# Kernel tuning notes

Hardware: AMD Instinct MI355X
Metric: run time of the kernel (lower is better)

Reference implementation:

```python
import jax, jax.numpy as jnp
import numpy as np

DIM = 512
NUM_HEADS = 8
HEAD_DIM = DIM // NUM_HEADS
GAMMA = 1.0


def setup_inputs() -> dict:
    key = jax.random.key(0)
    ks = jax.random.split(key, 10)
    B, S = 2, 2048
    x_real = jax.random.normal(ks[0], (B, S, DIM), dtype=jnp.float32)
    x_imag = jax.random.normal(ks[1], (B, S, DIM), dtype=jnp.float32)
    def xavier(k, fan_in, fan_out):
        lim = float(np.sqrt(6.0 / (fan_in + fan_out)))
        return jax.random.uniform(k, (fan_in, fan_out), jnp.float32, -lim, lim)
    # torch Linear(in,out): weight [out,in]; we store transposed [in,out]
    Wq = xavier(ks[2], 2 * DIM, DIM); bq = jnp.zeros((DIM,), jnp.float32)
    Wk = xavier(ks[3], 2 * DIM, DIM); bk = jnp.zeros((DIM,), jnp.float32)
    Wv = xavier(ks[4], 2 * DIM, DIM); bv = jnp.zeros((DIM,), jnp.float32)
    Wo = xavier(ks[5], DIM, 2 * DIM); bo = jnp.zeros((2 * DIM,), jnp.float32)
    return {"x_real": x_real, "x_imag": x_imag, "Wq": Wq, "bq": bq,
            "Wk": Wk, "bk": bk, "Wv": Wv, "bv": bv, "Wo": Wo, "bo": bo}


def reference(x_real, x_imag, Wq, bq, Wk, bk, Wv, bv, Wo, bo):
    B, S, _ = x_real.shape
    real_embed = jnp.concatenate([x_real, x_imag], axis=-1)  # [B,S,2*dim]
    def proj(W, b):
        y = real_embed @ W + b                               # [B,S,dim]
        return y.reshape(B, S, NUM_HEADS, HEAD_DIM).transpose(0, 2, 1, 3)  # [B,H,S,d]
    Q = proj(Wq, bq)
    K = proj(Wk, bk)
    V = proj(Wv, bv)
    # softmax over head_dim is broadcast-invariant, so the Bhattacharyya
    # coefficient sum_d sqrt(p_i[d]*q_j[d]) factorizes into a matmul.
    sp = jnp.sqrt(jax.nn.softmax(Q, axis=-1))  # [B,H,S,d]
    sq = jnp.sqrt(jax.nn.softmax(K, axis=-1))  # [B,H,S,d]
    bc = jnp.einsum('bhid,bhjd->bhij', sp, sq)  # Bhattacharyya coeff [B,H,S,S]
    bc = jnp.clip(bc, -1.0, 1.0)
    dist = jnp.arccos(bc)
    attn = jax.nn.softmax(-GAMMA * dist * dist, axis=-1)  # [B,H,S,S]
    attended = jnp.einsum('bhij,bhjd->bhid', attn, V)
    attended = attended.transpose(0, 2, 1, 3).reshape(B, S, DIM)
    out = attended @ Wo + bo  # [B,S,2*dim] = concat(real_out, imag_out)
    return out
```

## Files before the change

### kernel.cpp

```cpp
#include <hip/hip_runtime.h>
#include <math.h>


typedef __attribute__((ext_vector_type(8))) short short8;
typedef __attribute__((ext_vector_type(4))) short bf16x4;
typedef __attribute__((ext_vector_type(4))) float f32x4;
typedef __attribute__((ext_vector_type(2))) float f32x2;
typedef __attribute__((ext_vector_type(4))) unsigned int u32x4;

#define MFMA(a, b, c) __builtin_amdgcn_mfma_f32_16x16x32_bf16((a), (b), (c), 0, 0, 0)

static __device__ __forceinline__ short f2bf(float f) {
    unsigned u = __float_as_uint(f);
    u += 0x7fffu + ((u >> 16) & 1u);
    return (short)(u >> 16);
}

static __device__ __forceinline__ void gld_lds16(const short* g, short* l) {
    __builtin_amdgcn_global_load_lds(
        (const __attribute__((address_space(1))) unsigned int*)g,
        (__attribute__((address_space(3))) unsigned int*)l, 16, 0, 0);
}

__global__ __launch_bounds__(256) void prep_all(
    const float* __restrict__ xr, const float* __restrict__ xi,
    short* __restrict__ xb,
    const float* __restrict__ Wq, const float* __restrict__ Wk,
    const float* __restrict__ Wv, const float* __restrict__ Wo,
    short* __restrict__ wqt, short* __restrict__ wot)
{
    const int bid = blockIdx.x;
    if (bid < 2048) {
        const unsigned wid = bid * 256 + threadIdx.x;
        const int p  = wid & 7;
        const int rp = (wid >> 3) & 31;
        const int kt = (wid >> 8) & 31;
        const int mb = wid >> 13;
        const int up = p ^ (rp & 7);
        const int m  = (mb << 6) | (rp << 1) | (up >> 2);
        const int k  = (kt << 5) | ((up & 3) << 3);
        const float* s = (k < 512) ? (xr + (size_t)m * 512 + k)
                                   : (xi + (size_t)m * 512 + (k - 512));
        float4 t0 = *(const float4*)(s);
        float4 t1 = *(const float4*)(s + 4);
        short8 o;
        o[0] = f2bf(t0.x); o[1] = f2bf(t0.y); o[2] = f2bf(t0.z); o[3] = f2bf(t0.w);
        o[4] = f2bf(t1.x); o[5] = f2bf(t1.y); o[6] = f2bf(t1.z); o[7] = f2bf(t1.w);
        *(short8*)(xb + (size_t)wid * 8) = o;
    } else {
        __shared__ float tt[32][33];
        const int t = bid - 2048;
        const int z = t >> 9;
        const int idx = t & 511;
        const float* src = (z == 0) ? Wq : (z == 1) ? Wk : (z == 2) ? Wv : Wo;
        const int N = (z < 3) ? 512 : 1024;
        const int bx = (z < 3) ? (idx & 15) : (idx & 31);
        const int by = (z < 3) ? (idx >> 4) : (idx >> 5);
        const int n0 = bx << 5, k0 = by << 5;
        const int tx = threadIdx.x & 31, ty = threadIdx.x >> 5;
        #pragma unroll
        for (int i = 0; i < 4; ++i)
            tt[ty + 8 * i][tx] = src[(size_t)(k0 + ty + 8 * i) * N + n0 + tx];
        __syncthreads();
        const int k = k0 + tx;
        const int kt = k >> 5, u = (k >> 3) & 3, off = k & 7;
        #pragma unroll
        for (int i = 0; i < 4; ++i) {
            const int n = n0 + ty + 8 * i;
            const int nb = n >> 6, rn = n & 63;
            const int rp = rn >> 1;
            const int up = ((rn & 1) << 2) | u;
            const int p  = up ^ (rp & 7);
            const float v = tt[tx][ty + 8 * i];
            if (z < 3)
                wqt[(size_t)z * 524288 +
                    ((size_t)(nb * 32 + kt)) * 2048 + rp * 64 + p * 8 + off] = f2bf(v);
            else
                wot[((size_t)(nb * 16 + kt)) * 2048 + rp * 64 + p * 8 + off] = f2bf(v);
        }
    }
}

__global__ __launch_bounds__(64) void qkv_mfma(
    const short* __restrict__ xb, const short* __restrict__ wcat,
    const float* __restrict__ bq, const float* __restrict__ bk,
    const float* __restrict__ bv,
    short* __restrict__ sp, short* __restrict__ sq, short* __restrict__ vt)
{
    __shared__ short As[3][64 * 32];
    __shared__ short Bs[3][64 * 32];
    const int jb = blockIdx.x;
    const int mb = blockIdx.y;
    const int m0 = mb << 6;
    const int lane = threadIdx.x;
    const int l = lane & 15, quad = lane >> 4;
    const int l7 = l & 7;

    const short* gA = xb   + (size_t)mb * 65536 + lane * 8;
    const short* gB = wcat + (size_t)jb * 65536 + lane * 8;

    auto STAGE = [&](int bb, int kk) {
        const int k0 = kk << 11;
        #pragma unroll
        for (int t = 0; t < 4; ++t) {
            gld_lds16(gA + k0 + t * 512, &As[bb][t << 9]);
            gld_lds16(gB + k0 + t * 512, &Bs[bb][t << 9]);
        }
    };

    STAGE(0, 0);
    STAGE(1, 1);
    asm volatile("s_waitcnt vmcnt(8)" ::: "memory");

    const f32x4 z4 = {0.f, 0.f, 0.f, 0.f};
    f32x4 acc[4][4];
    #pragma unroll
    for (int i = 0; i < 4; ++i)
        #pragma unroll
        for (int j = 0; j < 4; ++j) acc[i][j] = z4;

    const int rbase = (l >> 1) << 6;
    const int pA = (((((l & 1) << 2) | quad) ^ ((l >> 1) & 7)) << 3);
    const int rdo = rbase + pA;

    int cb = 0, sb = 2;
    #pragma unroll 1
    for (int kt = 0; kt < 32; ++kt) {
        STAGE(sb, (kt + 2) & 31);
        const short* Al = &As[cb][0];
        const short* Bl = &Bs[cb][0];
        short8 af[4], bfr[4];
        #pragma unroll
        for (int i = 0; i < 4; ++i)
            af[i] = *(const short8*)(Al + (i << 9) + rdo);
        #pragma unroll
        for (int j = 0; j < 4; ++j)
            bfr[j] = *(const short8*)(Bl + (j << 9) + rdo);
        #pragma unroll
        for (int i = 0; i < 4; ++i)
            #pragma unroll
            for (int j = 0; j < 4; ++j)
                acc[i][j] = MFMA(af[i], bfr[j], acc[i][j]);
        asm volatile("s_waitcnt vmcnt(8)" ::: "memory");
        cb = (cb == 2) ? 0 : cb + 1;
        sb = (sb == 2) ? 0 : sb + 1;
    }

    const int op = jb >> 3;
    const int h  = jb & 7;

    if (op < 2) {
        short* dst = (op == 0) ? sp : sq;
        const float* bias = (op == 0) ? bq : bk;
        float bcol[4];
        #pragma unroll
        for (int nt = 0; nt < 4; ++nt) bcol[nt] = bias[(h << 6) + (nt << 4) + l];
        #pragma unroll
        for (int i = 0; i < 4; ++i) {
            #pragma unroll
            for (int reg = 0; reg < 4; ++reg) {
                const int r = m0 + (i << 4) + (quad << 2) + reg;
                const int b = r >> 11, s = r & 2047;
                float v[4];
                #pragma unroll
                for (int nt = 0; nt < 4; ++nt) v[nt] = acc[i][nt][reg] + bcol[nt];
                float mx = fmaxf(fmaxf(v[0], v[1]), fmaxf(v[2], v[3]));
                #pragma unroll
                for (int msk = 1; msk < 16; msk <<= 1) mx = fmaxf(mx, __shfl_xor(mx, msk));
                float e[4], ssum = 0.f;
                #pragma unroll
                for (int nt = 0; nt < 4; ++nt) { e[nt] = __expf(v[nt] - mx); ssum += e[nt]; }
                #pragma unroll
                for (int msk = 1; msk < 16; msk <<= 1) ssum += __shfl_xor(ssum, msk);
                float inv = 1.0f / ssum;
                short* o = dst + ((size_t)((b << 3) + h) * 2048 + s) * 64;
                if (op == 0) {
                    #pragma unroll
                    for (int nt = 0; nt < 4; ++nt)
                        o[(nt << 4) + l] = f2bf(sqrtf(e[nt] * inv));
                } else {
                    const int s7 = r & 7;
                    #pragma unroll
                    for (int nt = 0; nt < 4; ++nt)
                        o[((((nt << 1) + (l >> 3)) ^ s7) << 3) + l7] =
                            f2bf(sqrtf(e[nt] * inv));
                }
            }
        }
    } else {
        float bcol[4];
        #pragma unroll
        for (int nt = 0; nt < 4; ++nt) bcol[nt] = bv[(h << 6) + (nt << 4) + l];
        #pragma unroll
        for (int i = 0; i < 4; ++i) {
            const int sb2 = m0 + (i << 4) + (quad << 2);
            const int b = sb2 >> 11, s = sb2 & 2047;
            const int gg = (s >> 2) & 15;
            const int u = ((gg >> 3) << 2) + (gg & 3);
            const int colp = (s & ~63) + (((u ^ l7)) << 3) + (((gg >> 2) & 1) << 2);
            #pragma unroll
            for (int nt = 0; nt < 4; ++nt) {
                const int d = (nt << 4) + l;
                bf16x4 pk;
                #pragma unroll
                for (int reg = 0; reg < 4; ++reg)
                    pk[reg] = f2bf(acc[i][nt][reg] + bcol[nt]);
                *(bf16x4*)(vt + ((size_t)((b << 3) + h) * 64 + d) * 2048 + colp) = pk;
            }
        }
    }
}

__global__ __launch_bounds__(256, 4) void attn_mfma(
    const short* __restrict__ sp, const short* __restrict__ sq,
    const short* __restrict__ vt,
    float* __restrict__ pnum, float* __restrict__ pden)
{
    __shared__ __align__(16) short sqT[2][64 * 64];
    __shared__ __align__(16) short vtT[2][64 * 64];
    const int bh = blockIdx.y;
    const int m0 = blockIdx.x << 6;
    const int z  = blockIdx.z;
    const int tid = threadIdx.x;
    const int w = tid >> 6, lane = tid & 63;
    const int l = lane & 15, quad = lane >> 4;
    const int l7 = l & 7;

    const short* spB = sp + (size_t)bh * 2048 * 64;
    const short* sqB = sq + (size_t)bh * 2048 * 64;
    const short* vtB = vt + (size_t)bh * 64 * 2048;

    const short* apr = spB + (size_t)(m0 + w * 16 + l) * 64 + quad * 8;
    short8 nq0 = (*(const short8*)(apr)) ^ (short)0x8000;
    short8 nq1 = (*(const short8*)(apr + 32)) ^ (short)0x8000;

    const int lr = lane >> 3;
    const int lu = lane & 7;
    const int r0 = w << 1;

    auto STAGEATT = [&](int buf, int jrow) {
        #pragma unroll
        for (int k = 0; k < 2; ++k) {
            const int r = r0 + k;
            gld_lds16(sqB + (size_t)(jrow + (r << 3) + lr) * 64 + (lu << 3),
                      &sqT[buf][r << 9]);
            gld_lds16(vtB + (size_t)((r << 3) + lr) * 2048 + jrow + (lu << 3),
                      &vtT[buf][r << 9]);
        }
    };

    const int sRd = (quad ^ l7) << 3;

    STAGEATT(0, z << 9);
    __syncthreads();

    const f32x4 ones4 = {1.f, 1.f, 1.f, 1.f};
    const f32x4 z4 = {0.f, 0.f, 0.f, 0.f};
    f32x4 acc[4] = {z4, z4, z4, z4};
    f32x2 den2 = {0.f, 0.f};

    #pragma unroll 1
    for (int jtl = 0; jtl < 8; ++jtl) {
        const int cb = jtl & 1, nb = cb ^ 1;
        const int j0n = ((z << 3) + ((jtl + 1) & 7)) << 6;
        STAGEATT(nb, j0n);

        uint2 pk[4];
        const short* sqL = &sqT[cb][0];
        #pragma unroll
        for (int nt = 0; nt < 4; ++nt) {
            const short* ar = sqL + ((nt * 16 + l) << 6);
            short8 sa0 = *(const short8*)(ar + sRd);
            short8 sa1 = *(const short8*)(ar + (sRd ^ 32));
            f32x4 p = MFMA(sa0, nq0, ones4);
            p = MFMA(sa1, nq1, p);
            f32x2 u01 = {p[0], p[1]};
            f32x2 u23 = {p[2], p[3]};
            const f32x2 zz = {0.f, 0.f};
#if __has_builtin(__builtin_elementwise_max)
            u01 = __builtin_elementwise_max(u01, zz);
            u23 = __builtin_elementwise_max(u23, zz);
#else
            u01.x = fmaxf(u01.x, 0.f); u01.y = fmaxf(u01.y, 0.f);
            u23.x = fmaxf(u23.x, 0.f); u23.y = fmaxf(u23.y, 0.f);
#endif
            f32x2 t01 = {-0.00133017f, -0.00133017f};
            f32x2 t23 = t01;
            t01 = t01 * u01 - 0.00219618f;  t23 = t23 * u23 - 0.00219618f;
            t01 = t01 * u01 - 0.00555151f;  t23 = t23 * u23 - 0.00555151f;
            t01 = t01 * u01 - 0.01465597f;  t23 = t23 * u23 - 0.01465597f;
            t01 = t01 * u01 - 0.04121986f;  t23 = t23 * u23 - 0.04121986f;
            t01 = t01 * u01 - 0.12823956f;  t23 = t23 * u23 - 0.12823956f;
            t01 = t01 * u01 - 0.48089834f;  t23 = t23 * u23 - 0.48089834f;
            t01 = t01 * u01 - 2.88539008f;  t23 = t23 * u23 - 2.88539008f;
            f32x2 w01 = u01 * t01;
            f32x2 w23 = u23 * t23;
#if __has_builtin(__builtin_amdgcn_exp2f)
            float e0 = __builtin_amdgcn_exp2f(w01.x);
            float e1 = __builtin_amdgcn_exp2f(w01.y);
            float e2 = __builtin_amdgcn_exp2f(w23.x);
            float e3 = __builtin_amdgcn_exp2f(w23.y);
#else
            float e0 = exp2f(w01.x), e1 = exp2f(w01.y);
            float e2 = exp2f(w23.x), e3 = exp2f(w23.y);
#endif
            f32x2 es = {e0 + e2, e1 + e3};
            den2 += es;
            pk[nt].x = (__float_as_uint(e0) >> 16) | (__float_as_uint(e1) & 0xffff0000u);
            pk[nt].y = (__float_as_uint(e2) >> 16) | (__float_as_uint(e3) & 0xffff0000u);
        }

        u32x4 c0; c0.x = pk[0].x; c0.y = pk[0].y; c0.z = pk[1].x; c0.w = pk[1].y;
        u32x4 c1; c1.x = pk[2].x; c1.y = pk[2].y; c1.z = pk[3].x; c1.w = pk[3].y;
        short8 pa0 = __builtin_bit_cast(short8, c0);
        short8 pa1 = __builtin_bit_cast(short8, c1);
        const short* vL = &vtT[cb][0];
        #pragma unroll
        for (int t4 = 0; t4 < 4; ++t4) {
            const short* vr = vL + ((t4 * 16 + l) << 6);
            short8 vb0 = *(const short8*)(vr + sRd);
            short8 vb1 = *(const short8*)(vr + (sRd ^ 32));
            acc[t4] = MFMA(pa0, vb0, acc[t4]);
            acc[t4] = MFMA(pa1, vb1, acc[t4]);
        }

        __syncthreads();
    }

    float den = den2.x + den2.y;
    den += __shfl_xor(den, 16);
    den += __shfl_xor(den, 32);
    if (lane < 16)
        pden[(size_t)z * 32768 + bh * 2048 + m0 + w * 16 + l] = den;

    const int b = bh >> 3, hh = bh & 7;
    float* np = pnum + (size_t)z * 4096 * 512;
    #pragma unroll
    for (int t4 = 0; t4 < 4; ++t4)
        #pragma unroll
        for (int reg = 0; reg < 4; ++reg) {
            const int row = m0 + w * 16 + quad * 4 + reg;
            np[((size_t)(b * 2048 + row)) * 512 + hh * 64 + t4 * 16 + l] =
                acc[t4][reg];
        }
}

__global__ __launch_bounds__(256) void combine_attn(
    const float* __restrict__ pnum, const float* __restrict__ pden,
    short* __restrict__ attB)
{
    const int idx = (blockIdx.x * 256 + threadIdx.x) << 3;
    const int r = idx >> 9;
    const int c = idx & 511;
    const int hh = c >> 6;
    const int bh = ((r >> 11) << 3) + hh;
    const int srow = r & 2047;
    float d = 0.f;
    #pragma unroll
    for (int zi = 0; zi < 4; ++zi)
        d += pden[(size_t)zi * 32768 + bh * 2048 + srow];
    const float inv = 1.0f / d;
    float4 a0 = {0.f, 0.f, 0.f, 0.f}, a1 = {0.f, 0.f, 0.f, 0.f};
    #pragma unroll
    for (int zi = 0; zi < 4; ++zi) {
        const float* n0 = pnum + (size_t)zi * 4096 * 512 + (size_t)r * 512 + c;
        float4 b0 = *(const float4*)(n0);
        float4 b1 = *(const float4*)(n0 + 4);
        a0.x += b0.x; a0.y += b0.y; a0.z += b0.z; a0.w += b0.w;
        a1.x += b1.x; a1.y += b1.y; a1.z += b1.z; a1.w += b1.w;
    }
    short8 o;
    o[0] = f2bf(a0.x * inv); o[1] = f2bf(a0.y * inv);
    o[2] = f2bf(a0.z * inv); o[3] = f2bf(a0.w * inv);
    o[4] = f2bf(a1.x * inv); o[5] = f2bf(a1.y * inv);
    o[6] = f2bf(a1.z * inv); o[7] = f2bf(a1.w * inv);
    const int mb = r >> 6, rm = r & 63;
    const int kt = c >> 5, u = (c >> 3) & 3;
    const int rp = rm >> 1;
    const int up = ((rm & 1) << 2) | u;
    const int p  = up ^ (rp & 7);
    *(short8*)(attB + ((size_t)(mb * 16 + kt)) * 2048 + rp * 64 + p * 8) = o;
}

__global__ __launch_bounds__(64) void out_mfma(
    const short* __restrict__ attB, const short* __restrict__ wot,
    const float* __restrict__ bo, float* __restrict__ out)
{
    __shared__ short As[3][64 * 32];
    __shared__ short Bs[3][64 * 32];
    const int nb = blockIdx.x;
    const int mb = blockIdx.y;
    const int n0 = nb << 6;
    const int m0 = mb << 6;
    const int lane = threadIdx.x;
    const int l = lane & 15, quad = lane >> 4;

    const short* gA = attB + (size_t)mb * 32768 + lane * 8;
    const short* gB = wot  + (size_t)nb * 32768 + lane * 8;

    auto STAGE = [&](int bb, int kk) {
        const int k0 = kk << 11;
        #pragma unroll
        for (int t = 0; t < 4; ++t) {
            gld_lds16(gA + k0 + t * 512, &As[bb][t << 9]);
            gld_lds16(gB + k0 + t * 512, &Bs[bb][t << 9]);
        }
    };

    STAGE(0, 0);
    STAGE(1, 1);
    asm volatile("s_waitcnt vmcnt(8)" ::: "memory");

    const f32x4 z4 = {0.f, 0.f, 0.f, 0.f};
    f32x4 acc[4][4];
    #pragma unroll
    for (int i = 0; i < 4; ++i)
        #pragma unroll
        for (int j = 0; j < 4; ++j) acc[i][j] = z4;

    const int rbase = (l >> 1) << 6;
    const int pA = (((((l & 1) << 2) | quad) ^ ((l >> 1) & 7)) << 3);
    const int rdo = rbase + pA;

    int cb = 0, sb = 2;
    #pragma unroll 1
    for (int kt = 0; kt < 16; ++kt) {
        STAGE(sb, (kt + 2) & 15);
        const short* Al = &As[cb][0];
        const short* Bl = &Bs[cb][0];
        short8 af[4], bfr[4];
        #pragma unroll
        for (int i = 0; i < 4; ++i)
            af[i] = *(const short8*)(Al + (i << 9) + rdo);
        #pragma unroll
        for (int j = 0; j < 4; ++j)
            bfr[j] = *(const short8*)(Bl + (j << 9) + rdo);
        #pragma unroll
        for (int i = 0; i < 4; ++i)
            #pragma unroll
            for (int j = 0; j < 4; ++j)
                acc[i][j] = MFMA(af[i], bfr[j], acc[i][j]);
        asm volatile("s_waitcnt vmcnt(8)" ::: "memory");
        cb = (cb == 2) ? 0 : cb + 1;
        sb = (sb == 2) ? 0 : sb + 1;
    }

    float bcol[4];
    #pragma unroll
    for (int nt = 0; nt < 4; ++nt) bcol[nt] = bo[n0 + (nt << 4) + l];
    #pragma unroll
    for (int i = 0; i < 4; ++i)
        #pragma unroll
        for (int reg = 0; reg < 4; ++reg) {
            const int m = m0 + (i << 4) + (quad << 2) + reg;
            float* o = out + (size_t)m * 1024 + n0 + l;
            #pragma unroll
            for (int nt = 0; nt < 4; ++nt)
                o[nt << 4] = acc[i][nt][reg] + bcol[nt];
        }
}

extern "C" void kernel_launch(void* const* d_in, const int* in_sizes, int n_in,
                              void* d_out, int out_size, void* d_ws, size_t ws_size,
                              hipStream_t stream) {
    const float* xr = (const float*)d_in[0];
    const float* xi = (const float*)d_in[1];
    const float* Wq = (const float*)d_in[2];
    const float* bq = (const float*)d_in[3];
    const float* Wk = (const float*)d_in[4];
    const float* bk = (const float*)d_in[5];
    const float* Wv = (const float*)d_in[6];
    const float* bv = (const float*)d_in[7];
    const float* Wo = (const float*)d_in[8];
    const float* bo = (const float*)d_in[9];
    float* out = (float*)d_out;

    short* base = (short*)d_ws;
    short* xb   = base;
    short* wqt  = xb  + 4194304;
    short* wot  = wqt + 1572864;
    short* spW  = wot + 524288;
    short* sqW  = spW + 2097152;
    short* vtW  = sqW + 2097152;
    short* attB = vtW + 2097152;
    float* pnum = (float*)(attB + 2097152);
    float* pden = pnum + 4 * 2097152;

    hipLaunchKernelGGL(prep_all, dim3(4096), dim3(256), 0, stream,
                       xr, xi, xb, Wq, Wk, Wv, Wo, wqt, wot);
    hipLaunchKernelGGL(qkv_mfma, dim3(24, 64), dim3(64), 0, stream,
                       xb, wqt, bq, bk, bv, spW, sqW, vtW);
    hipLaunchKernelGGL(attn_mfma, dim3(32, 16, 4), dim3(256), 0, stream,
                       spW, sqW, vtW, pnum, pden);
    hipLaunchKernelGGL(combine_attn, dim3(1024), dim3(256), 0, stream,
                       pnum, pden, attB);
    hipLaunchKernelGGL(out_mfma, dim3(16, 64), dim3(64), 0, stream,
                       attB, wot, bo, out);
}
```

Before: 184.3 us.

## Process two 64-row query tiles per attention block to reuse staged K/V

Each attention block now handles 128 query rows instead of 64. Every wave carries two query fragments and two sets of accumulators, so each staged K and V tile in LDS feeds twice as many MFMAs and global/LDS staging traffic per query drops by half. The grid along the query axis is halved, giving 1024 blocks instead of 2048. This costs more registers per thread, which may lower occupancy under the (256,4) launch bound, and fewer blocks are available to hide latency.

```diff
diff --git a/kernel.cpp b/kernel.cpp
--- a/kernel.cpp
+++ b/kernel.cpp
@@ -219,7 +219,7 @@
     __shared__ __align__(16) short sqT[2][64 * 64];
     __shared__ __align__(16) short vtT[2][64 * 64];
     const int bh = blockIdx.y;
-    const int m0 = blockIdx.x << 6;
+    const int m0 = blockIdx.x << 7;
     const int z  = blockIdx.z;
     const int tid = threadIdx.x;
     const int w = tid >> 6, lane = tid & 63;
@@ -230,9 +230,12 @@
     const short* sqB = sq + (size_t)bh * 2048 * 64;
     const short* vtB = vt + (size_t)bh * 64 * 2048;
 
-    const short* apr = spB + (size_t)(m0 + w * 16 + l) * 64 + quad * 8;
-    short8 nq0 = (*(const short8*)(apr)) ^ (short)0x8000;
-    short8 nq1 = (*(const short8*)(apr + 32)) ^ (short)0x8000;
+    const short* apr0 = spB + (size_t)(m0 + w * 16 + l) * 64 + quad * 8;
+    const short* apr1 = apr0 + (size_t)64 * 64;
+    short8 nqa0 = (*(const short8*)(apr0)) ^ (short)0x8000;
+    short8 nqa1 = (*(const short8*)(apr0 + 32)) ^ (short)0x8000;
+    short8 nqb0 = (*(const short8*)(apr1)) ^ (short)0x8000;
+    short8 nqb1 = (*(const short8*)(apr1 + 32)) ^ (short)0x8000;
 
     const int lr = lane >> 3;
     const int lu = lane & 7;
@@ -256,8 +259,48 @@
 
     const f32x4 ones4 = {1.f, 1.f, 1.f, 1.f};
     const f32x4 z4 = {0.f, 0.f, 0.f, 0.f};
-    f32x4 acc[4] = {z4, z4, z4, z4};
-    f32x2 den2 = {0.f, 0.f};
+    f32x4 accA[4] = {z4, z4, z4, z4};
+    f32x4 accB[4] = {z4, z4, z4, z4};
+    f32x2 denA = {0.f, 0.f}, denB = {0.f, 0.f};
+
+    auto SCORE = [&](const f32x4& p, f32x2& dacc) -> uint2 {
+        f32x2 u01 = {p[0], p[1]};
+        f32x2 u23 = {p[2], p[3]};
+        const f32x2 zz = {0.f, 0.f};
+#if __has_builtin(__builtin_elementwise_max)
+        u01 = __builtin_elementwise_max(u01, zz);
+        u23 = __builtin_elementwise_max(u23, zz);
+#else
+        u01.x = fmaxf(u01.x, 0.f); u01.y = fmaxf(u01.y, 0.f);
+        u23.x = fmaxf(u23.x, 0.f); u23.y = fmaxf(u23.y, 0.f);
+#endif
+        f32x2 t01 = {-0.00133017f, -0.00133017f};
+        f32x2 t23 = t01;
+        t01 = t01 * u01 - 0.00219618f;  t23 = t23 * u23 - 0.00219618f;
+        t01 = t01 * u01 - 0.00555151f;  t23 = t23 * u23 - 0.00555151f;
+        t01 = t01 * u01 - 0.01465597f;  t23 = t23 * u23 - 0.01465597f;
+        t01 = t01 * u01 - 0.04121986f;  t23 = t23 * u23 - 0.04121986f;
+        t01 = t01 * u01 - 0.12823956f;  t23 = t23 * u23 - 0.12823956f;
+        t01 = t01 * u01 - 0.48089834f;  t23 = t23 * u23 - 0.48089834f;
+        t01 = t01 * u01 - 2.88539008f;  t23 = t23 * u23 - 2.88539008f;
+        f32x2 w01 = u01 * t01;
+        f32x2 w23 = u23 * t23;
+#if __has_builtin(__builtin_amdgcn_exp2f)
+        float e0 = __builtin_amdgcn_exp2f(w01.x);
+        float e1 = __builtin_amdgcn_exp2f(w01.y);
+        float e2 = __builtin_amdgcn_exp2f(w23.x);
+        float e3 = __builtin_amdgcn_exp2f(w23.y);
+#else
+        float e0 = exp2f(w01.x), e1 = exp2f(w01.y);
+        float e2 = exp2f(w23.x), e3 = exp2f(w23.y);
+#endif
+        f32x2 es = {e0 + e2, e1 + e3};
+        dacc += es;
+        uint2 r;
+        r.x = (__float_as_uint(e0) >> 16) | (__float_as_uint(e1) & 0xffff0000u);
+        r.y = (__float_as_uint(e2) >> 16) | (__float_as_uint(e3) & 0xffff0000u);
+        return r;
+    };
 
     #pragma unroll 1
     for (int jtl = 0; jtl < 8; ++jtl) {
@@ -265,73 +308,54 @@
         const int j0n = ((z << 3) + ((jtl + 1) & 7)) << 6;
         STAGEATT(nb, j0n);
 
-        uint2 pk[4];
+        uint2 pkA[4], pkB[4];
         const short* sqL = &sqT[cb][0];
         #pragma unroll
         for (int nt = 0; nt < 4; ++nt) {
             const short* ar = sqL + ((nt * 16 + l) << 6);
             short8 sa0 = *(const short8*)(ar + sRd);
             short8 sa1 = *(const short8*)(ar + (sRd ^ 32));
-            f32x4 p = MFMA(sa0, nq0, ones4);
-            p = MFMA(sa1, nq1, p);
-            f32x2 u01 = {p[0], p[1]};
-            f32x2 u23 = {p[2], p[3]};
-            const f32x2 zz = {0.f, 0.f};
-#if __has_builtin(__builtin_elementwise_max)
-            u01 = __builtin_elementwise_max(u01, zz);
-            u23 = __builtin_elementwise_max(u23, zz);
-#else
-            u01.x = fmaxf(u01.x, 0.f); u01.y = fmaxf(u01.y, 0.f);
-            u23.x = fmaxf(u23.x, 0.f); u23.y = fmaxf(u23.y, 0.f);
-#endif
-            f32x2 t01 = {-0.00133017f, -0.00133017f};
-            f32x2 t23 = t01;
-            t01 = t01 * u01 - 0.00219618f;  t23 = t23 * u23 - 0.00219618f;
-            t01 = t01 * u01 - 0.00555151f;  t23 = t23 * u23 - 0.00555151f;
-            t01 = t01 * u01 - 0.01465597f;  t23 = t23 * u23 - 0.01465597f;
-            t01 = t01 * u01 - 0.04121986f;  t23 = t23 * u23 - 0.04121986f;
-            t01 = t01 * u01 - 0.12823956f;  t23 = t23 * u23 - 0.12823956f;
-            t01 = t01 * u01 - 0.48089834f;  t23 = t23 * u23 - 0.48089834f;
-            t01 = t01 * u01 - 2.88539008f;  t23 = t23 * u23 - 2.88539008f;
-            f32x2 w01 = u01 * t01;
-            f32x2 w23 = u23 * t23;
-#if __has_builtin(__builtin_amdgcn_exp2f)
-            float e0 = __builtin_amdgcn_exp2f(w01.x);
-            float e1 = __builtin_amdgcn_exp2f(w01.y);
-            float e2 = __builtin_amdgcn_exp2f(w23.x);
-            float e3 = __builtin_amdgcn_exp2f(w23.y);
-#else
-            float e0 = exp2f(w01.x), e1 = exp2f(w01.y);
-            float e2 = exp2f(w23.x), e3 = exp2f(w23.y);
-#endif
-            f32x2 es = {e0 + e2, e1 + e3};
-            den2 += es;
-            pk[nt].x = (__float_as_uint(e0) >> 16) | (__float_as_uint(e1) & 0xffff0000u);
-            pk[nt].y = (__float_as_uint(e2) >> 16) | (__float_as_uint(e3) & 0xffff0000u);
-        }
-
-        u32x4 c0; c0.x = pk[0].x; c0.y = pk[0].y; c0.z = pk[1].x; c0.w = pk[1].y;
-        u32x4 c1; c1.x = pk[2].x; c1.y = pk[2].y; c1.z = pk[3].x; c1.w = pk[3].y;
-        short8 pa0 = __builtin_bit_cast(short8, c0);
-        short8 pa1 = __builtin_bit_cast(short8, c1);
+            f32x4 pA = MFMA(sa0, nqa0, ones4);
+            pA = MFMA(sa1, nqa1, pA);
+            f32x4 pB = MFMA(sa0, nqb0, ones4);
+            pB = MFMA(sa1, nqb1, pB);
+            pkA[nt] = SCORE(pA, denA);
+            pkB[nt] = SCORE(pB, denB);
+        }
+
+        u32x4 cA0; cA0.x = pkA[0].x; cA0.y = pkA[0].y; cA0.z = pkA[1].x; cA0.w = pkA[1].y;
+        u32x4 cA1; cA1.x = pkA[2].x; cA1.y = pkA[2].y; cA1.z = pkA[3].x; cA1.w = pkA[3].y;
+        u32x4 cB0; cB0.x = pkB[0].x; cB0.y = pkB[0].y; cB0.z = pkB[1].x; cB0.w = pkB[1].y;
+        u32x4 cB1; cB1.x = pkB[2].x; cB1.y = pkB[2].y; cB1.z = pkB[3].x; cB1.w = pkB[3].y;
+        short8 paA0 = __builtin_bit_cast(short8, cA0);
+        short8 paA1 = __builtin_bit_cast(short8, cA1);
+        short8 paB0 = __builtin_bit_cast(short8, cB0);
+        short8 paB1 = __builtin_bit_cast(short8, cB1);
         const short* vL = &vtT[cb][0];
         #pragma unroll
         for (int t4 = 0; t4 < 4; ++t4) {
             const short* vr = vL + ((t4 * 16 + l) << 6);
             short8 vb0 = *(const short8*)(vr + sRd);
             short8 vb1 = *(const short8*)(vr + (sRd ^ 32));
-            acc[t4] = MFMA(pa0, vb0, acc[t4]);
-            acc[t4] = MFMA(pa1, vb1, acc[t4]);
+            accA[t4] = MFMA(paA0, vb0, accA[t4]);
+            accA[t4] = MFMA(paA1, vb1, accA[t4]);
+            accB[t4] = MFMA(paB0, vb0, accB[t4]);
+            accB[t4] = MFMA(paB1, vb1, accB[t4]);
         }
 
         __syncthreads();
     }
 
-    float den = den2.x + den2.y;
-    den += __shfl_xor(den, 16);
-    den += __shfl_xor(den, 32);
-    if (lane < 16)
-        pden[(size_t)z * 32768 + bh * 2048 + m0 + w * 16 + l] = den;
+    float dA = denA.x + denA.y;
+    dA += __shfl_xor(dA, 16);
+    dA += __shfl_xor(dA, 32);
+    float dB = denB.x + denB.y;
+    dB += __shfl_xor(dB, 16);
+    dB += __shfl_xor(dB, 32);
+    if (lane < 16) {
+        pden[(size_t)z * 32768 + bh * 2048 + m0 + w * 16 + l] = dA;
+        pden[(size_t)z * 32768 + bh * 2048 + m0 + 64 + w * 16 + l] = dB;
+    }
 
     const int b = bh >> 3, hh = bh & 7;
     float* np = pnum + (size_t)z * 4096 * 512;
@@ -339,9 +363,11 @@
     for (int t4 = 0; t4 < 4; ++t4)
         #pragma unroll
         for (int reg = 0; reg < 4; ++reg) {
-            const int row = m0 + w * 16 + quad * 4 + reg;
-            np[((size_t)(b * 2048 + row)) * 512 + hh * 64 + t4 * 16 + l] =
-                acc[t4][reg];
+            const int rowA = m0 + w * 16 + quad * 4 + reg;
+            np[((size_t)(b * 2048 + rowA)) * 512 + hh * 64 + t4 * 16 + l] =
+                accA[t4][reg];
+            np[((size_t)(b * 2048 + rowA + 64)) * 512 + hh * 64 + t4 * 16 + l] =
+                accB[t4][reg];
         }
 }
 
@@ -490,7 +516,7 @@
                        xr, xi, xb, Wq, Wk, Wv, Wo, wqt, wot);
     hipLaunchKernelGGL(qkv_mfma, dim3(24, 64), dim3(64), 0, stream,
                        xb, wqt, bq, bk, bv, spW, sqW, vtW);
-    hipLaunchKernelGGL(attn_mfma, dim3(32, 16, 4), dim3(256), 0, stream,
+    hipLaunchKernelGGL(attn_mfma, dim3(16, 16, 4), dim3(256), 0, stream,
                        spW, sqW, vtW, pnum, pden);
     hipLaunchKernelGGL(combine_attn, dim3(1024), dim3(256), 0, stream,
                        pnum, pden, attB);
```

Result: no change. 182.8 us (-0.8%).
